# Optimization experiments

Measured on AMD Instinct MI355X. Metric: run time of the kernel, lower is better.

The kernel has to match this reference:

```python
import jax, jax.numpy as jnp
import numpy as np

OUTPUT_DIM = 2000
INPUT_DIM = 8192
N_COLS = 2000  # must equal OUTPUT_DIM so bias broadcasts over last dim as in the torch code
SPARSITY = 0.9
BLOCK = 4


def _apply_block_sparsity(weight, block=BLOCK, sparsity=SPARSITY, seed=1234):
    # Zero out 4x4 blocks with probability `sparsity`, mirroring apply_block_sparsity.
    rng = np.random.RandomState(seed)
    rb = (weight.shape[0] + block - 1) // block
    cb = (weight.shape[1] + block - 1) // block
    keep = (rng.rand(rb, cb) <= (1.0 - sparsity)).astype(np.float32)
    mask = np.kron(keep, np.ones((block, block), dtype=np.float32))
    return weight * mask[: weight.shape[0], : weight.shape[1]]


def setup_inputs() -> dict:
    key = jax.random.key(0)
    k_w, k_b, k_x = jax.random.split(key, 3)
    weight = np.asarray(jax.random.normal(k_w, (OUTPUT_DIM, INPUT_DIM), dtype=jnp.float32))
    weight = jnp.asarray(_apply_block_sparsity(weight))
    bias = jax.random.normal(k_b, (OUTPUT_DIM,), dtype=jnp.float32)
    x = jax.random.normal(k_x, (INPUT_DIM, N_COLS), dtype=jnp.float32)
    return {"weight": weight, "bias": bias, "x": x}


def reference(weight, bias, x):
    # [OUT, IN] @ [IN, N] -> [OUT, N]; bias [OUT] broadcasts over last dim (N == OUT here),
    # exactly matching torch.matmul(weight, x) + bias.
    return jnp.matmul(weight, x) + bias
```

## Files before the change

### kernel.cpp

```cpp
#include <hip/hip_runtime.h>

#define K_DIM 8192
#define M_REAL 2000
#define N_REAL 2000
#define M_PAD 2048
#define N_PAD 2048

#define BM 256
#define BN 256
#define BK 32
#define SPLITK 4
#define KSLAB (K_DIM / SPLITK)
#define NIT (KSLAB / BK)

typedef __bf16 bf16x8 __attribute__((ext_vector_type(8)));
typedef float f32x4 __attribute__((ext_vector_type(4)));
typedef float fvec4 __attribute__((ext_vector_type(4)));

#define RAW_BARRIER()  asm volatile("s_barrier" ::: "memory")
#define WAIT_VM4()     asm volatile("s_waitcnt vmcnt(4)" ::: "memory")
#define WAIT_VM0()     asm volatile("s_waitcnt vmcnt(0)" ::: "memory")

__device__ __forceinline__ unsigned short f2bf(float f) {
    union { float f; unsigned u; } v; v.f = f;
    unsigned r = v.u + 0x7FFFu + ((v.u >> 16) & 1u);
    return (unsigned short)(r >> 16);
}

__device__ __forceinline__ unsigned pk2(float a, float b) {
    return (unsigned)f2bf(a) | ((unsigned)f2bf(b) << 16);
}

__device__ __forceinline__ void async16(const void* g, void* l) {
    __builtin_amdgcn_global_load_lds((__attribute__((address_space(1))) void*)(g),
                                     (__attribute__((address_space(3))) void*)(l),
                                     16, 0, 0);
}

__global__ __launch_bounds__(256) void prep_w(const float* __restrict__ W,
                                              unsigned short* __restrict__ Wb) {
    unsigned tid = blockIdx.x * 256u + threadIdx.x;
#pragma unroll
    for (unsigned i = 0; i < 8; ++i) {
        unsigned e = (i * (1024u * 256u) + tid) * 8u;
        uint4 o = make_uint4(0u, 0u, 0u, 0u);
        if (e < (unsigned)(M_REAL * K_DIM)) {
            fvec4 f0 = __builtin_nontemporal_load((const fvec4*)(W + e));
            fvec4 f1 = __builtin_nontemporal_load((const fvec4*)(W + e + 4));
            o.x = pk2(f0.x, f0.y);
            o.y = pk2(f0.z, f0.w);
            o.z = pk2(f1.x, f1.y);
            o.w = pk2(f1.z, f1.w);
        }
        *(uint4*)(Wb + e) = o;
    }
}

__global__ __launch_bounds__(256) void prep_x(const float* __restrict__ X,
                                              unsigned short* __restrict__ XT) {
    __shared__ unsigned short T[64][130];
    int b = blockIdx.x;
    int k0 = (b & 63) << 7;
    int n0 = (b >> 6) << 6;
    int t = threadIdx.x;
    int c = t & 15;
    int r = t >> 4;
    int nl = c << 2;
    int n = n0 + nl;
    bool valid = (n < N_REAL);
#pragma unroll
    for (int p = 0; p < 4; ++p) {
        int kl = (r << 1) + (p << 5);
        fvec4 v0 = {0.f, 0.f, 0.f, 0.f};
        fvec4 v1 = {0.f, 0.f, 0.f, 0.f};
        if (valid) {
            v0 = __builtin_nontemporal_load((const fvec4*)(X + (k0 + kl) * N_REAL + n));
            v1 = __builtin_nontemporal_load((const fvec4*)(X + (k0 + kl + 1) * N_REAL + n));
        }
        *(unsigned*)&T[nl + 0][kl] = pk2(v0.x, v1.x);
        *(unsigned*)&T[nl + 1][kl] = pk2(v0.y, v1.y);
        *(unsigned*)&T[nl + 2][kl] = pk2(v0.z, v1.z);
        *(unsigned*)&T[nl + 3][kl] = pk2(v0.w, v1.w);
    }
    __syncthreads();
#pragma unroll
    for (int it = 0; it < 4; ++it) {
        int nl2 = r + (it << 4);
        int kl2 = c << 3;
        const unsigned* tp = (const unsigned*)&T[nl2][kl2];
        uint4 o;
        o.x = tp[0]; o.y = tp[1]; o.z = tp[2]; o.w = tp[3];
        *(uint4*)(XT + (((n0 + nl2) << 13) + k0 + kl2)) = o;
    }
}

__global__ __launch_bounds__(256) void prep_init(const float* __restrict__ bias,
                                                 float* __restrict__ out) {
    const int total = M_REAL * (N_REAL / 4);
    for (int i = blockIdx.x * 256 + threadIdx.x; i < total; i += 1024 * 256) {
        int m = i / (N_REAL / 4);
        int n4 = i - m * (N_REAL / 4);
        float4 bv = *(const float4*)(bias + (n4 << 2));
        *(float4*)(out + m * N_REAL + (n4 << 2)) = bv;
    }
}

__global__ __launch_bounds__(512, 2) void gemm_kernel(const unsigned short* __restrict__ Wb,
                                                      const unsigned short* __restrict__ XT,
                                                      float* __restrict__ out) {
    __shared__ __align__(16) unsigned short As[2][BM * BK];
    __shared__ __align__(16) unsigned short Bs[2][BN * BK];

    int f = blockIdx.x;
    int xcd = f & 7;
    int local = f >> 3;
    int bz = local & 3;
    int bx = (xcd & 3) * 2 + ((local >> 2) & 1);
    int by = (xcd >> 2) * 4 + (local >> 3);

    int t = threadIdx.x;
    int w = t >> 6;
    int l = t & 63;
    int wm = (w >> 2) * 128;
    int wn = (w & 3) * 64;
    int lane16 = l & 15;
    int quad = l >> 4;
    int m0 = by * BM;
    int n0 = bx * BN;
    int ks = bz * KSLAB;

    f32x4 acc[8][4] = {};

    int srow = l >> 2;
    int scol = (l & 3) * 8;
    int rb = w * 32;
    const unsigned short* gA0 = Wb + (long long)(m0 + rb + srow) * K_DIM + ks + scol;
    const unsigned short* gA1 = gA0 + 16LL * K_DIM;
    const unsigned short* gB0 = XT + (long long)(n0 + rb + srow) * K_DIM + ks + scol;
    const unsigned short* gB1 = gB0 + 16LL * K_DIM;

    async16(gA0, &As[0][rb * BK]);
    async16(gA1, &As[0][(rb + 16) * BK]);
    async16(gB0, &Bs[0][rb * BK]);
    async16(gB1, &Bs[0][(rb + 16) * BK]);
    gA0 += BK; gA1 += BK; gB0 += BK; gB1 += BK;

    for (int kt = 0; kt < NIT; ++kt) {
        int cur = kt & 1;
        if (kt + 1 < NIT) {
            int nxt = cur ^ 1;
            async16(gA0, &As[nxt][rb * BK]);
            async16(gA1, &As[nxt][(rb + 16) * BK]);
            async16(gB0, &Bs[nxt][rb * BK]);
            async16(gB1, &Bs[nxt][(rb + 16) * BK]);
            gA0 += BK; gA1 += BK; gB0 += BK; gB1 += BK;
            WAIT_VM4();
        } else {
            WAIT_VM0();
        }
        RAW_BARRIER();

        bf16x8 a[8], b[4];
#pragma unroll
        for (int i = 0; i < 8; ++i)
            a[i] = *(const bf16x8*)&As[cur][(wm + i * 16 + lane16) * BK + quad * 8];
#pragma unroll
        for (int j = 0; j < 4; ++j)
            b[j] = *(const bf16x8*)&Bs[cur][(wn + j * 16 + lane16) * BK + quad * 8];

#pragma unroll
        for (int i = 0; i < 8; ++i)
#pragma unroll
            for (int j = 0; j < 4; ++j)
                acc[i][j] = __builtin_amdgcn_mfma_f32_16x16x32_bf16(a[i], b[j], acc[i][j], 0, 0, 0);

        if (kt + 1 < NIT)
            RAW_BARRIER();
    }

#pragma unroll
    for (int j = 0; j < 4; ++j) {
        int n = n0 + wn + j * 16 + lane16;
        if (n >= N_REAL) continue;
#pragma unroll
        for (int i = 0; i < 8; ++i) {
            int mbase = m0 + wm + i * 16 + quad * 4;
#pragma unroll
            for (int r = 0; r < 4; ++r) {
                int m = mbase + r;
                if (m < M_REAL)
                    atomicAdd(&out[(long long)m * N_REAL + n], acc[i][j][r]);
            }
        }
    }
}

extern "C" void kernel_launch(void* const* d_in, const int* in_sizes, int n_in,
                              void* d_out, int out_size, void* d_ws, size_t ws_size,
                              hipStream_t stream) {
    const float* W    = (const float*)d_in[0];
    const float* bias = (const float*)d_in[1];
    const float* X    = (const float*)d_in[2];
    float* out = (float*)d_out;

    unsigned short* Wb = (unsigned short*)d_ws;
    unsigned short* XT = Wb + (long long)M_PAD * K_DIM;

    prep_w<<<1024, 256, 0, stream>>>(W, Wb);
    prep_x<<<2048, 256, 0, stream>>>(X, XT);
    prep_init<<<1024, 256, 0, stream>>>(bias, out);

    gemm_kernel<<<(N_PAD / BN) * (M_PAD / BM) * SPLITK, 512, 0, stream>>>(Wb, XT, out);
}
```

Baseline: 270.0 us.

## Merge prep kernels and deepen GEMM pipeline with swizzled 4-stage LDS ring

Fuses the three preprocessing kernels (weight bf16 cast, X transpose/cast, bias init) into one launch with block-range dispatch, removing two kernel launches. The GEMM moves from double buffering to a 4-stage LDS ring buffer with a 3-deep prefetch. It uses an XOR swizzle on global-to-LDS chunk placement to cut bank conflicts, and splits each K step into two half-phases with s_setprio around the MFMA bursts. LDS use doubles to 128 KB per block, which may limit occupancy to one block per CU despite launch_bounds(512,2), and the added barriers add sync overhead.

```diff
diff --git a/kernel.cpp b/kernel.cpp
--- a/kernel.cpp
+++ b/kernel.cpp
@@ -11,13 +11,19 @@
 #define BK 32
 #define SPLITK 4
 #define KSLAB (K_DIM / SPLITK)
-#define NIT (KSLAB / BK)
+#define NSTEP (KSLAB / BK)
+
+#define NB_W 1024
+#define NB_X 2048
+#define NB_I 256
 
 typedef __bf16 bf16x8 __attribute__((ext_vector_type(8)));
 typedef float f32x4 __attribute__((ext_vector_type(4)));
 typedef float fvec4 __attribute__((ext_vector_type(4)));
 
 #define RAW_BARRIER()  asm volatile("s_barrier" ::: "memory")
+#define LGKM0()        asm volatile("s_waitcnt lgkmcnt(0)" ::: "memory")
+#define WAIT_VM8()     asm volatile("s_waitcnt vmcnt(8)" ::: "memory")
 #define WAIT_VM4()     asm volatile("s_waitcnt vmcnt(4)" ::: "memory")
 #define WAIT_VM0()     asm volatile("s_waitcnt vmcnt(0)" ::: "memory")
 
@@ -37,79 +43,80 @@
                                      16, 0, 0);
 }
 
-__global__ __launch_bounds__(256) void prep_w(const float* __restrict__ W,
-                                              unsigned short* __restrict__ Wb) {
-    unsigned tid = blockIdx.x * 256u + threadIdx.x;
-#pragma unroll
-    for (unsigned i = 0; i < 8; ++i) {
-        unsigned e = (i * (1024u * 256u) + tid) * 8u;
-        uint4 o = make_uint4(0u, 0u, 0u, 0u);
-        if (e < (unsigned)(M_REAL * K_DIM)) {
-            fvec4 f0 = __builtin_nontemporal_load((const fvec4*)(W + e));
-            fvec4 f1 = __builtin_nontemporal_load((const fvec4*)(W + e + 4));
-            o.x = pk2(f0.x, f0.y);
-            o.y = pk2(f0.z, f0.w);
-            o.z = pk2(f1.x, f1.y);
-            o.w = pk2(f1.z, f1.w);
-        }
-        *(uint4*)(Wb + e) = o;
-    }
-}
-
-__global__ __launch_bounds__(256) void prep_x(const float* __restrict__ X,
-                                              unsigned short* __restrict__ XT) {
+__global__ __launch_bounds__(256) void prep_kernel(const float* __restrict__ W,
+                                                   const float* __restrict__ X,
+                                                   const float* __restrict__ bias,
+                                                   unsigned short* __restrict__ Wb,
+                                                   unsigned short* __restrict__ XT,
+                                                   float* __restrict__ out) {
     __shared__ unsigned short T[64][130];
-    int b = blockIdx.x;
-    int k0 = (b & 63) << 7;
-    int n0 = (b >> 6) << 6;
-    int t = threadIdx.x;
-    int c = t & 15;
-    int r = t >> 4;
-    int nl = c << 2;
-    int n = n0 + nl;
-    bool valid = (n < N_REAL);
-#pragma unroll
-    for (int p = 0; p < 4; ++p) {
-        int kl = (r << 1) + (p << 5);
-        fvec4 v0 = {0.f, 0.f, 0.f, 0.f};
-        fvec4 v1 = {0.f, 0.f, 0.f, 0.f};
-        if (valid) {
-            v0 = __builtin_nontemporal_load((const fvec4*)(X + (k0 + kl) * N_REAL + n));
-            v1 = __builtin_nontemporal_load((const fvec4*)(X + (k0 + kl + 1) * N_REAL + n));
-        }
-        *(unsigned*)&T[nl + 0][kl] = pk2(v0.x, v1.x);
-        *(unsigned*)&T[nl + 1][kl] = pk2(v0.y, v1.y);
-        *(unsigned*)&T[nl + 2][kl] = pk2(v0.z, v1.z);
-        *(unsigned*)&T[nl + 3][kl] = pk2(v0.w, v1.w);
-    }
-    __syncthreads();
-#pragma unroll
-    for (int it = 0; it < 4; ++it) {
-        int nl2 = r + (it << 4);
-        int kl2 = c << 3;
-        const unsigned* tp = (const unsigned*)&T[nl2][kl2];
-        uint4 o;
-        o.x = tp[0]; o.y = tp[1]; o.z = tp[2]; o.w = tp[3];
-        *(uint4*)(XT + (((n0 + nl2) << 13) + k0 + kl2)) = o;
-    }
-}
-
-__global__ __launch_bounds__(256) void prep_init(const float* __restrict__ bias,
-                                                 float* __restrict__ out) {
-    const int total = M_REAL * (N_REAL / 4);
-    for (int i = blockIdx.x * 256 + threadIdx.x; i < total; i += 1024 * 256) {
-        int m = i / (N_REAL / 4);
-        int n4 = i - m * (N_REAL / 4);
-        float4 bv = *(const float4*)(bias + (n4 << 2));
-        *(float4*)(out + m * N_REAL + (n4 << 2)) = bv;
+    int bid = blockIdx.x;
+    if (bid < NB_W) {
+        unsigned tid = bid * 256u + threadIdx.x;
+#pragma unroll
+        for (unsigned i = 0; i < 8; ++i) {
+            unsigned e = (i * (1024u * 256u) + tid) * 8u;
+            uint4 o = make_uint4(0u, 0u, 0u, 0u);
+            if (e < (unsigned)(M_REAL * K_DIM)) {
+                fvec4 f0 = __builtin_nontemporal_load((const fvec4*)(W + e));
+                fvec4 f1 = __builtin_nontemporal_load((const fvec4*)(W + e + 4));
+                o.x = pk2(f0.x, f0.y);
+                o.y = pk2(f0.z, f0.w);
+                o.z = pk2(f1.x, f1.y);
+                o.w = pk2(f1.z, f1.w);
+            }
+            *(uint4*)(Wb + e) = o;
+        }
+    } else if (bid < NB_W + NB_X) {
+        int b = bid - NB_W;
+        int k0 = (b & 63) << 7;
+        int n0 = (b >> 6) << 6;
+        int t = threadIdx.x;
+        int c = t & 15;
+        int r = t >> 4;
+        int nl = c << 2;
+        int n = n0 + nl;
+        bool valid = (n < N_REAL);
+#pragma unroll
+        for (int p = 0; p < 4; ++p) {
+            int kl = (r << 1) + (p << 5);
+            fvec4 v0 = {0.f, 0.f, 0.f, 0.f};
+            fvec4 v1 = {0.f, 0.f, 0.f, 0.f};
+            if (valid) {
+                v0 = __builtin_nontemporal_load((const fvec4*)(X + (k0 + kl) * N_REAL + n));
+                v1 = __builtin_nontemporal_load((const fvec4*)(X + (k0 + kl + 1) * N_REAL + n));
+            }
+            *(unsigned*)&T[nl + 0][kl] = pk2(v0.x, v1.x);
+            *(unsigned*)&T[nl + 1][kl] = pk2(v0.y, v1.y);
+            *(unsigned*)&T[nl + 2][kl] = pk2(v0.z, v1.z);
+            *(unsigned*)&T[nl + 3][kl] = pk2(v0.w, v1.w);
+        }
+        __syncthreads();
+#pragma unroll
+        for (int it = 0; it < 4; ++it) {
+            int nl2 = r + (it << 4);
+            int kl2 = c << 3;
+            const unsigned* tp = (const unsigned*)&T[nl2][kl2];
+            uint4 o;
+            o.x = tp[0]; o.y = tp[1]; o.z = tp[2]; o.w = tp[3];
+            *(uint4*)(XT + (((n0 + nl2) << 13) + k0 + kl2)) = o;
+        }
+    } else {
+        const int total = M_REAL * (N_REAL / 4);
+        for (int i = (bid - NB_W - NB_X) * 256 + (int)threadIdx.x; i < total; i += NB_I * 256) {
+            int m = i / (N_REAL / 4);
+            int n4 = i - m * (N_REAL / 4);
+            float4 bv = *(const float4*)(bias + (n4 << 2));
+            *(float4*)(out + m * N_REAL + (n4 << 2)) = bv;
+        }
     }
 }
 
 __global__ __launch_bounds__(512, 2) void gemm_kernel(const unsigned short* __restrict__ Wb,
                                                       const unsigned short* __restrict__ XT,
                                                       float* __restrict__ out) {
-    __shared__ __align__(16) unsigned short As[2][BM * BK];
-    __shared__ __align__(16) unsigned short Bs[2][BN * BK];
+    __shared__ __align__(16) unsigned short As[4][BM * BK];
+    __shared__ __align__(16) unsigned short Bs[4][BN * BK];
 
     int f = blockIdx.x;
     int xcd = f & 7;
@@ -131,52 +138,117 @@
 
     f32x4 acc[8][4] = {};
 
-    int srow = l >> 2;
-    int scol = (l & 3) * 8;
-    int rb = w * 32;
-    const unsigned short* gA0 = Wb + (long long)(m0 + rb + srow) * K_DIM + ks + scol;
-    const unsigned short* gA1 = gA0 + 16LL * K_DIM;
-    const unsigned short* gB0 = XT + (long long)(n0 + rb + srow) * K_DIM + ks + scol;
-    const unsigned short* gB1 = gB0 + 16LL * K_DIM;
-
-    async16(gA0, &As[0][rb * BK]);
-    async16(gA1, &As[0][(rb + 16) * BK]);
-    async16(gB0, &Bs[0][rb * BK]);
-    async16(gB1, &Bs[0][(rb + 16) * BK]);
-    gA0 += BK; gA1 += BK; gB0 += BK; gB1 += BK;
-
-    for (int kt = 0; kt < NIT; ++kt) {
-        int cur = kt & 1;
-        if (kt + 1 < NIT) {
-            int nxt = cur ^ 1;
-            async16(gA0, &As[nxt][rb * BK]);
-            async16(gA1, &As[nxt][(rb + 16) * BK]);
-            async16(gB0, &Bs[nxt][rb * BK]);
-            async16(gB1, &Bs[nxt][(rb + 16) * BK]);
-            gA0 += BK; gA1 += BK; gB0 += BK; gB1 += BK;
-            WAIT_VM4();
-        } else {
-            WAIT_VM0();
-        }
-        RAW_BARRIER();
-
-        bf16x8 a[8], b[4];
-#pragma unroll
-        for (int i = 0; i < 8; ++i)
-            a[i] = *(const bf16x8*)&As[cur][(wm + i * 16 + lane16) * BK + quad * 8];
-#pragma unroll
-        for (int j = 0; j < 4; ++j)
-            b[j] = *(const bf16x8*)&Bs[cur][(wn + j * 16 + lane16) * BK + quad * 8];
-
-#pragma unroll
-        for (int i = 0; i < 8; ++i)
-#pragma unroll
-            for (int j = 0; j < 4; ++j)
-                acc[i][j] = __builtin_amdgcn_mfma_f32_16x16x32_bf16(a[i], b[j], acc[i][j], 0, 0, 0);
-
-        if (kt + 1 < NIT)
-            RAW_BARRIER();
+    int rlin = t >> 2;
+    int ck = (t & 3) ^ (rlin & 3);
+    const unsigned short* gA0 = Wb + (long long)(m0 + rlin) * K_DIM + ks + ck * 8;
+    const unsigned short* gA1 = gA0 + 128LL * K_DIM;
+    const unsigned short* gB0 = XT + (long long)(n0 + rlin) * K_DIM + ks + ck * 8;
+    const unsigned short* gB1 = gB0 + 128LL * K_DIM;
+
+    char* smA = (char*)&As[0][0];
+    char* smB = (char*)&Bs[0][0];
+    int wslot = w * 1024;
+
+#define STAGE_A(OFF) do { \
+        async16(gA0, smA + (OFF) + wslot); \
+        async16(gA1, smA + (OFF) + 8192 + wslot); \
+        gA0 += BK; gA1 += BK; } while (0)
+#define STAGE_B(OFF) do { \
+        async16(gB0, smB + (OFF) + wslot); \
+        async16(gB1, smB + (OFF) + 8192 + wslot); \
+        gB0 += BK; gB1 += BK; } while (0)
+
+    int swz = ((quad ^ (lane16 & 3)) << 4);
+    int arow = (wm + lane16) * 64 + swz;
+    int brow = (wn + lane16) * 64 + swz;
+
+    STAGE_A(0);     STAGE_B(0);
+    STAGE_A(16384); STAGE_B(16384);
+    STAGE_A(32768); STAGE_B(32768);
+    WAIT_VM8();
+    RAW_BARRIER();
+
+    int cur = 0;
+    int stg = 49152;
+
+    bf16x8 a0, a1, a2, a3, b0, b1, b2, b3;
+
+    for (int s = 0; s < NSTEP; ++s) {
+        {
+            const char* ab = smA + cur + arow;
+            const char* bb = smB + cur + brow;
+            a0 = *(const bf16x8*)(ab);
+            a1 = *(const bf16x8*)(ab + 1024);
+            a2 = *(const bf16x8*)(ab + 2048);
+            a3 = *(const bf16x8*)(ab + 3072);
+            b0 = *(const bf16x8*)(bb);
+            b1 = *(const bf16x8*)(bb + 1024);
+            b2 = *(const bf16x8*)(bb + 2048);
+            b3 = *(const bf16x8*)(bb + 3072);
+            if (s < NSTEP - 3) STAGE_A(stg);
+            RAW_BARRIER();
+            LGKM0();
+            __builtin_amdgcn_s_setprio(1);
+            acc[0][0] = __builtin_amdgcn_mfma_f32_16x16x32_bf16(a0, b0, acc[0][0], 0, 0, 0);
+            acc[0][1] = __builtin_amdgcn_mfma_f32_16x16x32_bf16(a0, b1, acc[0][1], 0, 0, 0);
+            acc[0][2] = __builtin_amdgcn_mfma_f32_16x16x32_bf16(a0, b2, acc[0][2], 0, 0, 0);
+            acc[0][3] = __builtin_amdgcn_mfma_f32_16x16x32_bf16(a0, b3, acc[0][3], 0, 0, 0);
+            acc[1][0] = __builtin_amdgcn_mfma_f32_16x16x32_bf16(a1, b0, acc[1][0], 0, 0, 0);
+            acc[1][1] = __builtin_amdgcn_mfma_f32_16x16x32_bf16(a1, b1, acc[1][1], 0, 0, 0);
+            acc[1][2] = __builtin_amdgcn_mfma_f32_16x16x32_bf16(a1, b2, acc[1][2], 0, 0, 0);
+            acc[1][3] = __builtin_amdgcn_mfma_f32_16x16x32_bf16(a1, b3, acc[1][3], 0, 0, 0);
+            acc[2][0] = __builtin_amdgcn_mfma_f32_16x16x32_bf16(a2, b0, acc[2][0], 0, 0, 0);
+            acc[2][1] = __builtin_amdgcn_mfma_f32_16x16x32_bf16(a2, b1, acc[2][1], 0, 0, 0);
+            acc[2][2] = __builtin_amdgcn_mfma_f32_16x16x32_bf16(a2, b2, acc[2][2], 0, 0, 0);
+            acc[2][3] = __builtin_amdgcn_mfma_f32_16x16x32_bf16(a2, b3, acc[2][3], 0, 0, 0);
+            acc[3][0] = __builtin_amdgcn_mfma_f32_16x16x32_bf16(a3, b0, acc[3][0], 0, 0, 0);
+            acc[3][1] = __builtin_amdgcn_mfma_f32_16x16x32_bf16(a3, b1, acc[3][1], 0, 0, 0);
+            acc[3][2] = __builtin_amdgcn_mfma_f32_16x16x32_bf16(a3, b2, acc[3][2], 0, 0, 0);
+            acc[3][3] = __builtin_amdgcn_mfma_f32_16x16x32_bf16(a3, b3, acc[3][3], 0, 0, 0);
+            __builtin_amdgcn_s_setprio(0);
+            RAW_BARRIER();
+        }
+        {
+            const char* ab = smA + cur + arow + 4096;
+            a0 = *(const bf16x8*)(ab);
+            a1 = *(const bf16x8*)(ab + 1024);
+            a2 = *(const bf16x8*)(ab + 2048);
+            a3 = *(const bf16x8*)(ab + 3072);
+            if (s < NSTEP - 3) {
+                STAGE_B(stg);
+                WAIT_VM8();
+            } else if (s == NSTEP - 3) {
+                WAIT_VM4();
+            } else if (s == NSTEP - 2) {
+                WAIT_VM0();
+            }
+            RAW_BARRIER();
+            LGKM0();
+            __builtin_amdgcn_s_setprio(1);
+            acc[4][0] = __builtin_amdgcn_mfma_f32_16x16x32_bf16(a0, b0, acc[4][0], 0, 0, 0);
+            acc[4][1] = __builtin_amdgcn_mfma_f32_16x16x32_bf16(a0, b1, acc[4][1], 0, 0, 0);
+            acc[4][2] = __builtin_amdgcn_mfma_f32_16x16x32_bf16(a0, b2, acc[4][2], 0, 0, 0);
+            acc[4][3] = __builtin_amdgcn_mfma_f32_16x16x32_bf16(a0, b3, acc[4][3], 0, 0, 0);
+            acc[5][0] = __builtin_amdgcn_mfma_f32_16x16x32_bf16(a1, b0, acc[5][0], 0, 0, 0);
+            acc[5][1] = __builtin_amdgcn_mfma_f32_16x16x32_bf16(a1, b1, acc[5][1], 0, 0, 0);
+            acc[5][2] = __builtin_amdgcn_mfma_f32_16x16x32_bf16(a1, b2, acc[5][2], 0, 0, 0);
+            acc[5][3] = __builtin_amdgcn_mfma_f32_16x16x32_bf16(a1, b3, acc[5][3], 0, 0, 0);
+            acc[6][0] = __builtin_amdgcn_mfma_f32_16x16x32_bf16(a2, b0, acc[6][0], 0, 0, 0);
+            acc[6][1] = __builtin_amdgcn_mfma_f32_16x16x32_bf16(a2, b1, acc[6][1], 0, 0, 0);
+            acc[6][2] = __builtin_amdgcn_mfma_f32_16x16x32_bf16(a2, b2, acc[6][2], 0, 0, 0);
+            acc[6][3] = __builtin_amdgcn_mfma_f32_16x16x32_bf16(a2, b3, acc[6][3], 0, 0, 0);
+            acc[7][0] = __builtin_amdgcn_mfma_f32_16x16x32_bf16(a3, b0, acc[7][0], 0, 0, 0);
+            acc[7][1] = __builtin_amdgcn_mfma_f32_16x16x32_bf16(a3, b1, acc[7][1], 0, 0, 0);
+            acc[7][2] = __builtin_amdgcn_mfma_f32_16x16x32_bf16(a3, b2, acc[7][2], 0, 0, 0);
+            acc[7][3] = __builtin_amdgcn_mfma_f32_16x16x32_bf16(a3, b3, acc[7][3], 0, 0, 0);
+            __builtin_amdgcn_s_setprio(0);
+            RAW_BARRIER();
+        }
+        cur = (cur + 16384) & 65535;
+        stg = (stg + 16384) & 65535;
     }
+#undef STAGE_A
+#undef STAGE_B
 
 #pragma unroll
     for (int j = 0; j < 4; ++j) {
@@ -206,9 +278,7 @@
     unsigned short* Wb = (unsigned short*)d_ws;
     unsigned short* XT = Wb + (long long)M_PAD * K_DIM;
 
-    prep_w<<<1024, 256, 0, stream>>>(W, Wb);
-    prep_x<<<2048, 256, 0, stream>>>(X, XT);
-    prep_init<<<1024, 256, 0, stream>>>(bias, out);
+    prep_kernel<<<NB_W + NB_X + NB_I, 256, 0, stream>>>(W, X, bias, Wb, XT, out);
 
     gemm_kernel<<<(N_PAD / BN) * (M_PAD / BM) * SPLITK, 512, 0, stream>>>(Wb, XT, out);
 }
```

After: 260.3 us. -3.6%, faster.
